# Kernel optimization log

Hardware: AMD Instinct MI355X
Metric: run time of the kernel (lower is better)

Reference implementation:

```python
import jax, jax.numpy as jnp
import numpy as np

DIM = 768   # embedding dim
NH = 12     # num heads
HD = DIM // NH  # head dim = 64
WS = 14     # window size
EPS = 1e-5  # nn.LayerNorm default


def _ln(x, w, b):
    m = jnp.mean(x, -1, keepdims=True)
    v = jnp.var(x, -1, keepdims=True)
    return (x - m) * jax.lax.rsqrt(v + EPS) * w + b


def setup_inputs() -> dict:
    key = jax.random.key(0)
    ks = jax.random.split(key, 8)
    def n(k, shape, s=0.02):
        return jax.random.normal(k, shape, jnp.float32) * s
    return {
        "x": jax.random.normal(ks[0], (4, 64, 64, DIM), jnp.float32),
        "ln1_w": jnp.ones((DIM,), jnp.float32),
        "ln1_b": jnp.zeros((DIM,), jnp.float32),
        "qkv_w": n(ks[1], (DIM, 3 * DIM)),
        "qkv_b": jnp.zeros((3 * DIM,), jnp.float32),
        "proj_w": n(ks[2], (DIM, DIM)),
        "proj_b": jnp.zeros((DIM,), jnp.float32),
        "rel_pos_h": n(ks[3], (2 * WS - 1, HD)),
        "rel_pos_w": n(ks[4], (2 * WS - 1, HD)),
        "ln2_w": jnp.ones((DIM,), jnp.float32),
        "ln2_b": jnp.zeros((DIM,), jnp.float32),
        "fc1_w": n(ks[5], (DIM, 4 * DIM)),
        "fc1_b": jnp.zeros((4 * DIM,), jnp.float32),
        "fc2_w": n(ks[6], (4 * DIM, DIM)),
        "fc2_b": jnp.zeros((DIM,), jnp.float32),
    }


def _block(x, ln1_w, ln1_b, qkv_w, qkv_b, proj_w, proj_b,
           rel_pos_h, rel_pos_w, ln2_w, ln2_b, fc1_w, fc1_b, fc2_w, fc2_b):
    B, H, W, C = x.shape
    shortcut = x
    xn = _ln(x, ln1_w, ln1_b)

    # ---- window partition (pad H,W up to multiples of WS) ----
    pad_h = (-H) % WS
    pad_w = (-W) % WS
    xp = jnp.pad(xn, ((0, 0), (0, pad_h), (0, pad_w), (0, 0)))
    Hp, Wp = H + pad_h, W + pad_w
    nh, nw = Hp // WS, Wp // WS
    xw = xp.reshape(B, nh, WS, nw, WS, C).transpose(0, 1, 3, 2, 4, 5)
    xw = xw.reshape(B * nh * nw, WS, WS, C)  # [Bw, ws, ws, C]
    Bw = B * nh * nw
    N = WS * WS

    # ---- attention with decomposed relative position bias ----
    qkv = xw.reshape(Bw, N, C) @ qkv_w + qkv_b            # [Bw, N, 3C]
    qkv = qkv.reshape(Bw, N, 3, NH, HD).transpose(2, 0, 3, 1, 4)  # [3, Bw, NH, N, HD]
    q, k, v = qkv[0], qkv[1], qkv[2]
    scale = HD ** -0.5
    attn = jnp.einsum("bhnd,bhmd->bhnm", q * scale, k)    # [Bw, NH, N, N]

    # decomposed rel pos: Rh[q_h, k_h, c], Rw[q_w, k_w, c]
    idx = jnp.arange(WS)[:, None] - jnp.arange(WS)[None, :] + (WS - 1)
    Rh = rel_pos_h[idx]  # [ws, ws, HD]
    Rw = rel_pos_w[idx]  # [ws, ws, HD]
    rq = q.reshape(Bw, NH, WS, WS, HD)
    rel_h = jnp.einsum("bnhwc,hkc->bnhwk", rq, Rh)  # over q rows vs k rows
    rel_w = jnp.einsum("bnhwc,wkc->bnhwk", rq, Rw)  # over q cols vs k cols
    attn = (attn.reshape(Bw, NH, WS, WS, WS, WS)
            + rel_h[..., :, None] + rel_w[..., None, :]).reshape(Bw, NH, N, N)

    attn = jax.nn.softmax(attn, axis=-1)
    out = jnp.einsum("bhnm,bhmd->bhnd", attn, v)          # [Bw, NH, N, HD]
    out = out.transpose(0, 2, 1, 3).reshape(Bw, WS, WS, C)
    out = out @ proj_w + proj_b

    # ---- window unpartition + crop padding ----
    out = out.reshape(B, nh, nw, WS, WS, C).transpose(0, 1, 3, 2, 4, 5)
    out = out.reshape(B, Hp, Wp, C)[:, :H, :W, :]

    x = shortcut + out

    # ---- MLP ----
    h = _ln(x, ln2_w, ln2_b)
    h = jax.nn.gelu(h @ fc1_w + fc1_b, approximate=False)
    x = x + (h @ fc2_w + fc2_b)
    return x


def reference(x, ln1_w, ln1_b, qkv_w, qkv_b, proj_w, proj_b,
              rel_pos_h, rel_pos_w, ln2_w, ln2_b, fc1_w, fc1_b, fc2_w, fc2_b):
    return _block(x, ln1_w, ln1_b, qkv_w, qkv_b, proj_w, proj_b,
                  rel_pos_h, rel_pos_w, ln2_w, ln2_b, fc1_w, fc1_b, fc2_w, fc2_b)
```

## Files before the change

### kernel.cpp

```cpp
#include <hip/hip_runtime.h>

typedef unsigned short u16;
typedef __bf16 bf16x8_t __attribute__((ext_vector_type(8)));
typedef float f32x4_t __attribute__((ext_vector_type(4)));

__device__ __forceinline__ float bf2f(u16 u) {
    union { unsigned u; float f; } c; c.u = ((unsigned)u) << 16; return c.f;
}
__device__ __forceinline__ u16 f2bf(float f) {
    union { float f; unsigned u; } c; c.f = f;
    unsigned u = c.u;
    unsigned r = (u + 0x7FFFu + ((u >> 16) & 1u)) >> 16;
    return (u16)r;
}

__device__ __forceinline__ void gld16(const u16* g, u16* l) {
    __builtin_amdgcn_global_load_lds(
        (const __attribute__((address_space(1))) unsigned*)g,
        (__attribute__((address_space(3))) unsigned*)l, 16, 0, 0);
}

__device__ __forceinline__ void block_sum2(float& s, float& sq) {
    for (int o = 32; o > 0; o >>= 1) { s += __shfl_xor(s, o); sq += __shfl_xor(sq, o); }
    __shared__ float sh[8];
    int wid = threadIdx.x >> 6;
    if ((threadIdx.x & 63) == 0) { sh[wid] = s; sh[4 + wid] = sq; }
    __syncthreads();
    s  = sh[0] + sh[1] + sh[2] + sh[3];
    sq = sh[4] + sh[5] + sh[6] + sh[7];
}

__global__ __launch_bounds__(256) void ln1_window(
    const float* __restrict__ x, const float* __restrict__ w, const float* __restrict__ b,
    u16* __restrict__ out, int row0)
{
    int lrow = blockIdx.x, tid = threadIdx.x;
    int wr = row0 + lrow;
    int wb = wr / 196, t = wr % 196;
    int gh = ((wb % 25) / 5) * 14 + t / 14;
    int gw = (wb % 5) * 14 + t % 14;
    size_t orow = (size_t)lrow * 768;
    __shared__ u16 rowbuf[768];
    if (gh >= 64 || gw >= 64) {
        rowbuf[tid] = 0; rowbuf[tid + 256] = 0; rowbuf[tid + 512] = 0;
        __syncthreads();
        if (tid < 96) *(uint4*)&out[orow + (tid << 3)] = *(const uint4*)&rowbuf[tid << 3];
        return;
    }
    size_t base = (size_t)(((wb / 25) * 64 + gh) * 64 + gw) * 768;
    float v0 = x[base + tid], v1 = x[base + tid + 256], v2 = x[base + tid + 512];
    float s = v0 + v1 + v2, sq = v0 * v0 + v1 * v1 + v2 * v2;
    block_sum2(s, sq);
    float mean = s * (1.0f / 768.0f);
    float var  = sq * (1.0f / 768.0f) - mean * mean;
    float inv  = rsqrtf(var + 1e-5f);
    rowbuf[tid]       = f2bf((v0 - mean) * inv * w[tid]       + b[tid]);
    rowbuf[tid + 256] = f2bf((v1 - mean) * inv * w[tid + 256] + b[tid + 256]);
    rowbuf[tid + 512] = f2bf((v2 - mean) * inv * w[tid + 512] + b[tid + 512]);
    __syncthreads();
    if (tid < 96) *(uint4*)&out[orow + (tid << 3)] = *(const uint4*)&rowbuf[tid << 3];
}

__global__ __launch_bounds__(256) void ln2_chunk(
    const float* __restrict__ xin, const float* __restrict__ w, const float* __restrict__ b,
    u16* __restrict__ out)
{
    int row = blockIdx.x, tid = threadIdx.x;
    size_t base = (size_t)row * 768;
    __shared__ u16 rowbuf[768];
    float v0 = xin[base + tid], v1 = xin[base + tid + 256], v2 = xin[base + tid + 512];
    float s = v0 + v1 + v2, sq = v0 * v0 + v1 * v1 + v2 * v2;
    block_sum2(s, sq);
    float mean = s * (1.0f / 768.0f);
    float var  = sq * (1.0f / 768.0f) - mean * mean;
    float inv  = rsqrtf(var + 1e-5f);
    rowbuf[tid]       = f2bf((v0 - mean) * inv * w[tid]       + b[tid]);
    rowbuf[tid + 256] = f2bf((v1 - mean) * inv * w[tid + 256] + b[tid + 256]);
    rowbuf[tid + 512] = f2bf((v2 - mean) * inv * w[tid + 512] + b[tid + 512]);
    __syncthreads();
    if (tid < 96) *(uint4*)&out[base + (tid << 3)] = *(const uint4*)&rowbuf[tid << 3];
}

__global__ __launch_bounds__(256) void transpose_wf(
    const float* __restrict__ in, u16* __restrict__ out, int K, int N)
{
    __shared__ u16 t[32][33];
    __shared__ u16 tt[32][32];
    int n0 = blockIdx.x * 32, k0 = blockIdx.y * 32;
    int tx = threadIdx.x & 31, ty = threadIdx.x >> 5;
    for (int q = 0; q < 4; q++) {
        int k = k0 + ty + q * 8, n = n0 + tx;
        t[ty + q * 8][tx] = (k < K && n < N) ? f2bf(in[(size_t)k * N + n]) : (u16)0;
    }
    __syncthreads();
    for (int q = 0; q < 4; q++) tt[ty + q * 8][tx] = t[tx][ty + q * 8];
    __syncthreads();
    if (threadIdx.x < 128) {
        int r = threadIdx.x >> 2, c8 = (threadIdx.x & 3) << 3;
        int n = n0 + r, k = k0 + c8;
        if (n < N && k < K)
            *(uint4*)&out[(size_t)n * K + k] = *(const uint4*)&tt[r][c8];
    }
}

__global__ __launch_bounds__(256) void build_relT(
    const float* __restrict__ rh, const float* __restrict__ rw, u16* __restrict__ out)
{
    int i = blockIdx.x * 256 + threadIdx.x;
    int r = i >> 6, c = i & 63;
    float v = (r < 27) ? rh[r * 64 + c] : (r < 54 ? rw[(r - 27) * 64 + c] : 0.f);
    out[i] = f2bf(v);
}

__global__ __launch_bounds__(256) void build_vt(
    const u16* __restrict__ qkvc, u16* __restrict__ vt)
{
    int z = blockIdx.x;
    int wb = z / 12, h = z % 12;
    __shared__ u16 t[64][232];
    int tid = threadIdx.x;
    for (int base = 0; base < 196; base += 4) {
        int m = base + (tid >> 6);
        int d = tid & 63;
        t[d][m] = qkvc[(size_t)(wb * 196 + m) * 2304 + 1536 + h * 64 + d];
    }
    for (int idx = tid; idx < 28 * 64; idx += 256) {
        int m = 196 + idx / 64, d = idx % 64;
        t[d][m] = 0;
    }
    __syncthreads();
    size_t ob = (size_t)z * 64 * 224;
    for (int idx = tid; idx < 64 * 28; idx += 256) {
        int d = idx / 28, c8 = (idx % 28) << 3;
        *(uint4*)&vt[ob + (size_t)d * 224 + c8] = *(const uint4*)&t[d][c8];
    }
}

__global__ __launch_bounds__(256) void softmax_rel2(
    u16* __restrict__ S, const u16* __restrict__ G2)
{
    int z = blockIdx.y;
    int wv = threadIdx.x >> 6, lane = threadIdx.x & 63;
    int n = blockIdx.x * 4 + wv;
    size_t srow = (size_t)z * 196 * 224 + (size_t)n * 224;
    const u16* g2 = G2 + (size_t)z * 196 * 64 + (size_t)n * 64;
    int qh = n / 14, qw = n % 14;
    float s[4];
    for (int c = 0; c < 4; c++) {
        int m = c * 64 + lane;
        if (m < 196) {
            int kk = m / 14, jj = m % 14;
            float bh = bf2f(g2[qh - kk + 13]);
            float bw = bf2f(g2[27 + qw - jj + 13]);
            s[c] = 0.125f * bf2f(S[srow + m]) + bh + bw;
        } else s[c] = -1e30f;
    }
    float mx = fmaxf(fmaxf(s[0], s[1]), fmaxf(s[2], s[3]));
    for (int o = 32; o > 0; o >>= 1) mx = fmaxf(mx, __shfl_xor(mx, o));
    float e[4], sm = 0.f;
    for (int c = 0; c < 4; c++) {
        int m = c * 64 + lane;
        e[c] = (m < 196) ? expf(s[c] - mx) : 0.f;
        sm += e[c];
    }
    for (int o = 32; o > 0; o >>= 1) sm += __shfl_xor(sm, o);
    float inv = 1.0f / sm;
    for (int c = 0; c < 4; c++) {
        int m = c * 64 + lane;
        if (m < 224) S[srow + m] = f2bf(e[c] * inv);
    }
}

__device__ __forceinline__ int swz_off(int row, int kcElem) {
    return row * 32 + (kcElem ^ (((row >> 1) & 3) << 3));
}

template <int MODE>
__global__ __launch_bounds__(256, 4) void gemm_nt(
    const u16* __restrict__ Aall, const u16* __restrict__ Ball,
    const float* __restrict__ bias, const float* xf,
    u16* __restrict__ Cb, float* Cf, int M, int row0)
{
    constexpr int BK = 32;
    int N, K, lda, ldb;
    size_t aoff = 0, boff = 0, coff = 0;
    if constexpr (MODE == 0) { N = 2304; K = 768; lda = 768; ldb = 768; }
    else if constexpr (MODE == 1) {
        N = 196; K = 64; lda = 2304; ldb = 2304;
        int z = blockIdx.z;
        aoff = (size_t)(z / 12) * 196 * 2304 + (size_t)(z % 12) * 64;
        boff = aoff + 768;
        coff = (size_t)z * 196 * 224;
    } else if constexpr (MODE == 2) {
        N = 64; K = 224; lda = 224; ldb = 224;
        int z = blockIdx.z;
        aoff = (size_t)z * 196 * 224;
        boff = (size_t)z * 64 * 224;
        coff = (size_t)(z / 12) * 196 * 768 + (size_t)(z % 12) * 64;
    } else if constexpr (MODE == 3) { N = 768; K = 768; lda = 768; ldb = 768; }
    else if constexpr (MODE == 4) { N = 3072; K = 768; lda = 768; ldb = 768; }
    else if constexpr (MODE == 6) {
        N = 64; K = 64; lda = 2304; ldb = 64;
        int z = blockIdx.z;
        aoff = (size_t)(z / 12) * 196 * 2304 + (size_t)(z % 12) * 64;
        boff = 0;
        coff = (size_t)z * 196 * 64;
    }
    else { N = 768; K = 3072; lda = 3072; ldb = 3072; }

    __shared__ __align__(16) u16 smem[8704];
    u16* As = smem;
    u16* Bs = smem + 4096;

    int tid = threadIdx.x, wid = tid >> 6, lane = tid & 63;
    int quad = lane >> 4, l16 = lane & 15;

    int bx = blockIdx.x, by = blockIdx.y;
    if constexpr (MODE != 1 && MODE != 2 && MODE != 6) {
        int gX = gridDim.x;
        int nwg = gX * gridDim.y;
        int orig = by * gX + bx;
        int q = nwg >> 3, r = nwg & 7;
        int xcd = orig & 7, idx = orig >> 3;
        int wg = (xcd < r ? xcd * (q + 1) : r * (q + 1) + (xcd - r) * q) + idx;
        bx = wg % gX; by = wg / gX;
    }
    int m_tile = by * 128, n_tile = bx * 128;
    int wm0 = (wid >> 1) * 64, wn0 = (wid & 1) * 64;

    const u16* A = Aall + aoff;
    const u16* B = Ball + boff;

    const u16* gA[2]; const u16* gB[2];
    u16 *lA[2], *lB[2];
    {
        int s = lane & 3, rofs = lane >> 2;
        for (int j = 0; j < 2; j++) {
            int r0 = wid * 32 + j * 16;
            int rr = r0 + rofs;
            int xr = (rr >> 1) & 3;
            int colo = ((s ^ xr) << 3);
            int am = m_tile + rr; if (am > M - 1) am = M - 1;
            int bn = n_tile + rr; if (bn > N - 1) bn = N - 1;
            gA[j] = A + (size_t)am * lda + colo;
            gB[j] = B + (size_t)bn * ldb + colo;
            lA[j] = &As[r0 * 32];
            lB[j] = &Bs[r0 * 32];
        }
    }

    f32x4_t acc[4][4];
    f32x4_t z4 = {0.f, 0.f, 0.f, 0.f};
    for (int mt = 0; mt < 4; mt++)
        for (int nt = 0; nt < 4; nt++) acc[mt][nt] = z4;

    for (int k0 = 0; k0 < K; k0 += BK) {
        gld16(gA[0] + k0, lA[0]);
        gld16(gA[1] + k0, lA[1]);
        gld16(gB[0] + k0, lB[0]);
        gld16(gB[1] + k0, lB[1]);
        __syncthreads();
        bf16x8_t af[4], bfv[4];
        for (int t = 0; t < 4; t++) {
            int ar = wm0 + t * 16 + l16;
            int br = wn0 + t * 16 + l16;
            af[t]  = *(const bf16x8_t*)&As[swz_off(ar, quad * 8)];
            bfv[t] = *(const bf16x8_t*)&Bs[swz_off(br, quad * 8)];
        }
        for (int mt = 0; mt < 4; mt++)
            for (int nt = 0; nt < 4; nt++)
                acc[mt][nt] = __builtin_amdgcn_mfma_f32_16x16x32_bf16(
                    af[mt], bfv[nt], acc[mt][nt], 0, 0, 0);
        __syncthreads();
    }

    if constexpr (MODE == 0 || MODE == 1 || MODE == 2 || MODE == 4 || MODE == 6) {
        u16* Cs = smem;
        int ldc = (MODE == 0) ? 2304 : (MODE == 1) ? 224 : (MODE == 2) ? 768
                : (MODE == 6) ? 64 : 3072;
        int colmax = (MODE == 1) ? 224 : N;
        for (int half = 0; half < 2; half++) {
            __syncthreads();
            if ((wm0 >> 6) == half) {
                for (int mt = 0; mt < 4; mt++) {
                    int rl = mt * 16 + quad * 4;
                    for (int nt = 0; nt < 4; nt++) {
                        int cl = wn0 + nt * 16 + l16;
                        int col = n_tile + cl;
                        for (int rg = 0; rg < 4; rg++) {
                            float v = acc[mt][nt][rg];
                            u16 o;
                            if constexpr (MODE == 0) o = f2bf(v + bias[col]);
                            else if constexpr (MODE == 4) {
                                float g = v + bias[col];
                                o = f2bf(0.5f * g * (1.0f + erff(g * 0.70710678118f)));
                            } else o = f2bf(v);
                            Cs[(rl + rg) * 136 + cl] = o;
                        }
                    }
                }
            }
            __syncthreads();
            for (int it = 0; it < 4; it++) {
                int chunk = tid + it * 256;
                int r = chunk >> 4, c8 = (chunk & 15) << 3;
                int grow = m_tile + half * 64 + r, gcol = n_tile + c8;
                if (grow >= M || gcol >= colmax) continue;
                *(uint4*)&Cb[coff + (size_t)grow * ldc + gcol] =
                    *(const uint4*)&Cs[r * 136 + c8];
            }
        }
    } else {
        float* Cfs = (float*)smem;
        for (int q = 0; q < 4; q++) {
            __syncthreads();
            if ((wm0 >> 6) == (q >> 1)) {
                for (int mt2 = 0; mt2 < 2; mt2++) {
                    int mt = (q & 1) * 2 + mt2;
                    int rloc = mt2 * 16 + quad * 4;
                    for (int nt = 0; nt < 4; nt++) {
                        int cl = wn0 + nt * 16 + l16;
                        for (int rg = 0; rg < 4; rg++)
                            Cfs[(rloc + rg) * 132 + cl] = acc[mt][nt][rg];
                    }
                }
            }
            __syncthreads();
            for (int it = 0; it < 4; it++) {
                int chunk = tid + it * 256;
                int r = chunk >> 5, c4 = (chunk & 31) << 2;
                int grow = m_tile + q * 32 + r;
                int gcol = n_tile + c4;
                if (grow >= M || gcol >= N) continue;
                f32x4_t v4 = *(const f32x4_t*)&Cfs[r * 132 + c4];
                f32x4_t b4 = *(const f32x4_t*)&bias[gcol];
                if constexpr (MODE == 5) {
                    size_t idx = (size_t)(row0 + grow) * 768 + gcol;
                    f32x4_t x4 = *(const f32x4_t*)&xf[idx];
                    f32x4_t o4;
                    for (int j = 0; j < 4; j++) o4[j] = v4[j] + x4[j] + b4[j];
                    *(f32x4_t*)&Cf[idx] = o4;
                } else {
                    int wr = row0 + grow;
                    int wb2 = wr / 196, t2 = wr % 196;
                    int gh = ((wb2 % 25) / 5) * 14 + t2 / 14;
                    int gw = (wb2 % 5) * 14 + t2 % 14;
                    if (gh < 64 && gw < 64) {
                        size_t g = (size_t)(((wb2 / 25) * 64 + gh) * 64 + gw) * 768 + gcol;
                        f32x4_t x4 = *(const f32x4_t*)&xf[g];
                        f32x4_t o4;
                        for (int j = 0; j < 4; j++) o4[j] = v4[j] + x4[j] + b4[j];
                        *(f32x4_t*)&Cf[g] = o4;
                    }
                }
            }
        }
    }
}

extern "C" void kernel_launch(void* const* d_in, const int* in_sizes, int n_in,
                              void* d_out, int out_size, void* d_ws, size_t ws_size,
                              hipStream_t stream)
{
    (void)in_sizes; (void)n_in; (void)out_size;
    const float* x      = (const float*)d_in[0];
    const float* ln1_w  = (const float*)d_in[1];
    const float* ln1_b  = (const float*)d_in[2];
    const float* qkv_w  = (const float*)d_in[3];
    const float* qkv_b  = (const float*)d_in[4];
    const float* proj_w = (const float*)d_in[5];
    const float* proj_b = (const float*)d_in[6];
    const float* rel_h  = (const float*)d_in[7];
    const float* rel_w  = (const float*)d_in[8];
    const float* ln2_w  = (const float*)d_in[9];
    const float* ln2_b  = (const float*)d_in[10];
    const float* fc1_w  = (const float*)d_in[11];
    const float* fc1_b  = (const float*)d_in[12];
    const float* fc2_w  = (const float*)d_in[13];
    const float* fc2_b  = (const float*)d_in[14];

    const size_t WT = 14155776ull + 8192ull;
    char* ws = (char*)d_ws;
    u16* qkvT  = (u16*)ws;
    u16* projT = qkvT + 2304 * 768;
    u16* fc1T  = projT + 768 * 768;
    u16* fc2T  = fc1T + 3072 * 768;
    u16* relT  = fc2T + 3072 * 768;
    char* scratch = ws + WT;
    size_t avail = (ws_size > WT) ? (ws_size - WT) : 0;

    const size_t perW = 3204096ull;
    static const int wc_cand[8] = {100, 50, 25, 20, 10, 5, 2, 1};
    int Wc = 1;
    for (int i = 0; i < 8; i++) {
        if ((size_t)wc_cand[i] * perW <= avail) { Wc = wc_cand[i]; break; }
    }
    static const int rm_cand[8] = {16384, 8192, 4096, 2048, 1024, 512, 256, 128};
    int Rm = 128;
    for (int i = 0; i < 8; i++) {
        if ((size_t)rm_cand[i] * 7680ull <= avail) { Rm = rm_cand[i]; break; }
    }

    u16* lnwc  = (u16*)scratch;
    u16* qkvc  = (u16*)(scratch + (size_t)Wc * 301056ull);
    u16* Sc    = (u16*)(scratch + (size_t)Wc * 1204224ull);
    u16* vtc   = (u16*)(scratch + (size_t)Wc * 2257920ull);
    u16* attnc = (u16*)(scratch + (size_t)Wc * 2601984ull);
    u16* G2c   = (u16*)(scratch + (size_t)Wc * 2903040ull);
    u16* hbuf  = (u16*)scratch;
    u16* xn2c  = (u16*)(scratch + (size_t)Rm * 6144ull);
    float* dout = (float*)d_out;

    transpose_wf<<<dim3(72, 24), 256, 0, stream>>>(qkv_w, qkvT, 768, 2304);
    transpose_wf<<<dim3(24, 24), 256, 0, stream>>>(proj_w, projT, 768, 768);
    transpose_wf<<<dim3(96, 24), 256, 0, stream>>>(fc1_w, fc1T, 768, 3072);
    transpose_wf<<<dim3(24, 96), 256, 0, stream>>>(fc2_w, fc2T, 3072, 768);
    build_relT<<<16, 256, 0, stream>>>(rel_h, rel_w, relT);

    int nch = 100 / Wc;
    int rows = Wc * 196;
    int gy = (rows + 127) / 128;
    for (int c = 0; c < nch; c++) {
        int r0 = c * rows;
        ln1_window<<<rows, 256, 0, stream>>>(x, ln1_w, ln1_b, lnwc, r0);
        gemm_nt<0><<<dim3(18, gy), 256, 0, stream>>>(
            lnwc, qkvT, qkv_b, nullptr, qkvc, nullptr, rows, 0);
        gemm_nt<1><<<dim3(2, 2, Wc * 12), 256, 0, stream>>>(
            qkvc, qkvc, nullptr, nullptr, Sc, nullptr, 196, 0);
        gemm_nt<6><<<dim3(1, 2, Wc * 12), 256, 0, stream>>>(
            qkvc, relT, nullptr, nullptr, G2c, nullptr, 196, 0);
        build_vt<<<Wc * 12, 256, 0, stream>>>(qkvc, vtc);
        softmax_rel2<<<dim3(49, Wc * 12), 256, 0, stream>>>(Sc, G2c);
        gemm_nt<2><<<dim3(1, 2, Wc * 12), 256, 0, stream>>>(
            Sc, vtc, nullptr, nullptr, attnc, nullptr, 196, 0);
        gemm_nt<3><<<dim3(6, gy), 256, 0, stream>>>(
            attnc, projT, proj_b, x, nullptr, dout, rows, r0);
    }

    int nm = 16384 / Rm;
    for (int c = 0; c < nm; c++) {
        int r0 = c * Rm;
        ln2_chunk<<<Rm, 256, 0, stream>>>(dout + (size_t)r0 * 768, ln2_w, ln2_b, xn2c);
        gemm_nt<4><<<dim3(24, Rm / 128), 256, 0, stream>>>(
            xn2c, fc1T, fc1_b, nullptr, hbuf, nullptr, Rm, 0);
        gemm_nt<5><<<dim3(6, Rm / 128), 256, 0, stream>>>(
            hbuf, fc2T, fc2_b, dout, nullptr, dout, Rm, r0);
    }
}
```

Baseline: 758.9 us.

## Double-buffer LDS tiles in the GEMM main loop to prefetch the next K slice

Shared memory grows to hold two A/B tile buffers. The kernel prefetches the first K slice before the loop, then each iteration issues the global-to-LDS loads for the next slice into the alternate buffer before computing on the current one. One of the two barriers per iteration is dropped. The aim is to hide global load latency behind the MFMA work, at the cost of roughly doubling LDS per block, which could lower occupancy.

```diff
diff --git a/kernel.cpp b/kernel.cpp
--- a/kernel.cpp
+++ b/kernel.cpp
@@ -208,9 +208,7 @@
     }
     else { N = 768; K = 3072; lda = 3072; ldb = 3072; }
 
-    __shared__ __align__(16) u16 smem[8704];
-    u16* As = smem;
-    u16* Bs = smem + 4096;
+    __shared__ __align__(16) u16 smem[16384];
 
     int tid = threadIdx.x, wid = tid >> 6, lane = tid & 63;
     int quad = lane >> 4, l16 = lane & 15;
@@ -232,7 +230,7 @@
     const u16* B = Ball + boff;
 
     const u16* gA[2]; const u16* gB[2];
-    u16 *lA[2], *lB[2];
+    int loff[2];
     {
         int s = lane & 3, rofs = lane >> 2;
         for (int j = 0; j < 2; j++) {
@@ -244,8 +242,7 @@
             int bn = n_tile + rr; if (bn > N - 1) bn = N - 1;
             gA[j] = A + (size_t)am * lda + colo;
             gB[j] = B + (size_t)bn * ldb + colo;
-            lA[j] = &As[r0 * 32];
-            lB[j] = &Bs[r0 * 32];
+            loff[j] = r0 * 32;
         }
     }
 
@@ -254,24 +251,36 @@
     for (int mt = 0; mt < 4; mt++)
         for (int nt = 0; nt < 4; nt++) acc[mt][nt] = z4;
 
+    for (int j = 0; j < 2; j++) {
+        gld16(gA[j], smem + loff[j]);
+        gld16(gB[j], smem + 4096 + loff[j]);
+    }
+
+    int cur = 0;
     for (int k0 = 0; k0 < K; k0 += BK) {
-        gld16(gA[0] + k0, lA[0]);
-        gld16(gA[1] + k0, lA[1]);
-        gld16(gB[0] + k0, lB[0]);
-        gld16(gB[1] + k0, lB[1]);
         __syncthreads();
+        int boffc = cur << 13;
+        if (k0 + BK < K) {
+            int boffn = boffc ^ 8192;
+            for (int j = 0; j < 2; j++) {
+                gld16(gA[j] + k0 + BK, smem + boffn + loff[j]);
+                gld16(gB[j] + k0 + BK, smem + boffn + 4096 + loff[j]);
+            }
+        }
+        const u16* Ac = smem + boffc;
+        const u16* Bc = smem + boffc + 4096;
         bf16x8_t af[4], bfv[4];
         for (int t = 0; t < 4; t++) {
             int ar = wm0 + t * 16 + l16;
             int br = wn0 + t * 16 + l16;
-            af[t]  = *(const bf16x8_t*)&As[swz_off(ar, quad * 8)];
-            bfv[t] = *(const bf16x8_t*)&Bs[swz_off(br, quad * 8)];
+            af[t]  = *(const bf16x8_t*)&Ac[swz_off(ar, quad * 8)];
+            bfv[t] = *(const bf16x8_t*)&Bc[swz_off(br, quad * 8)];
         }
         for (int mt = 0; mt < 4; mt++)
             for (int nt = 0; nt < 4; nt++)
                 acc[mt][nt] = __builtin_amdgcn_mfma_f32_16x16x32_bf16(
                     af[mt], bfv[nt], acc[mt][nt], 0, 0, 0);
-        __syncthreads();
+        cur ^= 1;
     }
 
     if constexpr (MODE == 0 || MODE == 1 || MODE == 2 || MODE == 4 || MODE == 6) {
```

Result: no change. 754.1 us (-0.6%).
